# Kernel tuning notes

Measured on AMD Instinct MI355X. Metric: run time of the kernel, lower is better.

## Reference

```python
import jax, jax.numpy as jnp
import numpy as np

NODE_DIM = 128
CTX_DIM = 256
OUT_DIM = 256
GRID_SIZE = 4
SPLINE_ORDER = 3
IN_DIM = 3 * NODE_DIM  # subj + obj + transformed context
N_NODES = 100000
N_EDGES = 100000


def make_grid(in_dim, grid_size, spline_order, grid_range=(-1.0, 1.0)):
    h = (grid_range[1] - grid_range[0]) / grid_size
    g = (np.arange(-spline_order, grid_size + spline_order + 1, dtype=np.float32) * h
         + grid_range[0])  # [grid_size + 2*spline_order + 1]
    return jnp.asarray(np.tile(g[None, :], (in_dim, 1)))  # [in, G]


def b_splines(x, grid, spline_order):
    # x: [N, in], grid: [in, G] -> bases: [N, in, grid_size + spline_order]
    xg = x[:, :, None]
    bases = ((xg >= grid[:, :-1]) & (xg < grid[:, 1:])).astype(x.dtype)
    for k in range(1, spline_order + 1):
        left = (xg - grid[:, : -(k + 1)]) / (grid[:, k:-1] - grid[:, : -(k + 1)]) * bases[..., :-1]
        right = (grid[:, k + 1:] - xg) / (grid[:, k + 1:] - grid[:, 1:-k]) * bases[..., 1:]
        bases = left + right
    return bases


def setup_inputs() -> dict:
    key = jax.random.key(0)
    ks = jax.random.split(key, 8)
    n_coef = GRID_SIZE + SPLINE_ORDER
    return {
        "node_embeddings": jax.random.normal(ks[0], (N_NODES, NODE_DIM), jnp.float32),
        "context_embeddings": jax.random.normal(ks[1], (N_EDGES, CTX_DIM), jnp.float32),
        "pair_indices": jax.random.randint(ks[2], (N_EDGES, 2), 0, N_NODES, jnp.int64 if jax.config.jax_enable_x64 else jnp.int32),
        "ctx_w": jax.random.normal(ks[3], (NODE_DIM, CTX_DIM), jnp.float32) * (1.0 / np.sqrt(CTX_DIM)),
        "ctx_b": jnp.zeros((NODE_DIM,), jnp.float32),
        "base_weight": jax.random.normal(ks[4], (OUT_DIM, IN_DIM), jnp.float32) * (1.0 / np.sqrt(IN_DIM)),
        "spline_weight": jax.random.normal(ks[5], (OUT_DIM, IN_DIM, n_coef), jnp.float32) * 0.1,
        "spline_scaler": jax.random.normal(ks[6], (OUT_DIM, IN_DIM), jnp.float32) * (1.0 / np.sqrt(IN_DIM)),
        "grid": make_grid(IN_DIM, GRID_SIZE, SPLINE_ORDER),
    }


def reference(node_embeddings, context_embeddings, pair_indices, ctx_w, ctx_b,
              base_weight, spline_weight, spline_scaler, grid):
    # gather subject/object node embeddings (irregular access)
    subj = node_embeddings[pair_indices[:, 0]]          # [E, node_dim]
    obj = node_embeddings[pair_indices[:, 1]]           # [E, node_dim]
    ctx = context_embeddings @ ctx_w.T + ctx_b          # [E, node_dim]
    x = jnp.concatenate([subj, obj, ctx], axis=1)       # [E, 3*node_dim]

    # efficient-KAN linear layer: base (SiLU) branch + B-spline branch
    base_out = jax.nn.silu(x) @ base_weight.T           # [E, out]
    bsp = b_splines(x, grid, SPLINE_ORDER)              # [E, in, n_coef]
    scaled_w = spline_weight * spline_scaler[:, :, None]  # [out, in, n_coef]
    spline_out = jnp.einsum('nic,oic->no', bsp, scaled_w)
    return base_out + spline_out
```

## Files before the change

### kernel.cpp

```cpp
#include <hip/hip_runtime.h>

#define NEDGES   100000
#define NODE_DIM 128
#define CTX_DIM  256
#define OUT_DIM  256
#define IN_DIM   384
#define NCOEF    7

#define BM2      128
#define BK2      32
#define NCH2     96
#define THR2     512

typedef __bf16 bf16x8 __attribute__((ext_vector_type(8)));
typedef float  f32x4  __attribute__((ext_vector_type(4)));

static __device__ __forceinline__ unsigned short f2bf(float f) {
    unsigned int u = __float_as_uint(f);
    u += 0x7FFFu + ((u >> 16) & 1u);
    return (unsigned short)(u >> 16);
}
static __device__ __forceinline__ float bf2f(unsigned short h) {
    return __uint_as_float(((unsigned int)h) << 16);
}
static __device__ __forceinline__ unsigned int pkbf(float a, float b) {
    unsigned int ua = __float_as_uint(a), ub = __float_as_uint(b);
    ua += 0x7FFFu + ((ua >> 16) & 1u);
    ub += 0x7FFFu + ((ub >> 16) & 1u);
    return (ua >> 16) | (ub & 0xFFFF0000u);
}
static __device__ __forceinline__ float silu(float x) {
    return x / (1.0f + __expf(-x));
}
static __device__ __forceinline__ float n3(float t) {
    float d2 = t - 2.0f;
    float a  = fabsf(d2);
    float p1 = fmaf(fmaf(0.5f, a, -1.0f), d2 * d2, 0.66666667f);
    float dd = fmaxf(2.0f - a, 0.0f);
    float p2 = dd * dd * (dd * (1.0f / 6.0f));
    return a < 1.0f ? p1 : p2;
}

static __device__ __forceinline__ void glds16(const unsigned short* g, unsigned short* l) {
    __builtin_amdgcn_global_load_lds(
        (const __attribute__((address_space(1))) void*)g,
        (__attribute__((address_space(3))) void*)l, 16, 0, 0);
}

__global__ void prep_w2(const float* __restrict__ base_w,
                        const float* __restrict__ spline_w,
                        const float* __restrict__ spline_s,
                        unsigned short* __restrict__ Wsw)
{
    int o = blockIdx.x;
    int i = threadIdx.x;
    int bi = o * IN_DIM + i;
    float sc = spline_s[bi];
    const float* sw = spline_w + (size_t)bi * NCOEF;
    uint4 v;
    v.x = pkbf(base_w[bi], sw[0] * sc);
    v.y = pkbf(sw[1] * sc, sw[2] * sc);
    v.z = pkbf(sw[3] * sc, sw[4] * sc);
    v.w = pkbf(sw[5] * sc, sw[6] * sc);
    int ch = i >> 2, g8 = i & 3;
    int p  = o * 4 + (((o >> 1) + g8) & 3);
    *(uint4*)(Wsw + (size_t)ch * (OUT_DIM * BK2) + p * 8) = v;
}

__global__ void prep_ctxw(const float* __restrict__ ctx_w,
                          unsigned short* __restrict__ B)
{
    int n  = blockIdx.x;
    int k4 = threadIdx.x;
    float4 v = *(const float4*)(ctx_w + (size_t)n * CTX_DIM + k4 * 4);
    *(uint2*)&B[(size_t)n * CTX_DIM + k4 * 4] =
        make_uint2(pkbf(v.x, v.y), pkbf(v.z, v.w));
}

#define CG_STR 72
#define CG_ESTR 136
__global__ __launch_bounds__(512, 4)
void ctx_gemm(const float* __restrict__ ctx_emb,
              const unsigned short* __restrict__ ctxwB,
              const float* __restrict__ ctx_b,
              unsigned short* __restrict__ CtxB)
{
    __shared__ unsigned short sm[2 * 128 * CG_STR];
    const int tid    = threadIdx.x;
    const int e_base = blockIdx.x * 128;
    const int wid    = tid >> 6;
    const int lan    = tid & 63;
    const int lrow   = lan & 15;
    const int lquad  = lan >> 4;
    const int m0     = (wid & 1) * 64;
    const int n0     = (wid >> 1) * 32;

    f32x4 acc[4][2];
    #pragma unroll
    for (int a = 0; a < 4; ++a)
        #pragma unroll
        for (int b = 0; b < 2; ++b) { f32x4 z = {0.f,0.f,0.f,0.f}; acc[a][b] = z; }

    #pragma unroll
    for (int it = 0; it < 4; ++it) {
        int id = it * 512 + tid;
        int r  = id >> 4;
        int c4 = id & 15;
        int eg = e_base + r; if (eg >= NEDGES) eg = NEDGES - 1;
        float4 v = *(const float4*)(ctx_emb + (size_t)eg * CTX_DIM + c4 * 4);
        *(uint2*)&sm[r * CG_STR + c4 * 4] = make_uint2(pkbf(v.x, v.y), pkbf(v.z, v.w));
    }
    __syncthreads();

    for (int kc = 0; kc < 4; ++kc) {
        if (kc + 1 < 4) {
            unsigned short* nb = sm + ((kc + 1) & 1) * 128 * CG_STR;
            #pragma unroll
            for (int it = 0; it < 4; ++it) {
                int id = it * 512 + tid;
                int r  = id >> 4;
                int c4 = id & 15;
                int eg = e_base + r; if (eg >= NEDGES) eg = NEDGES - 1;
                float4 v = *(const float4*)(ctx_emb + (size_t)eg * CTX_DIM + (kc + 1) * 64 + c4 * 4);
                *(uint2*)&nb[r * CG_STR + c4 * 4] = make_uint2(pkbf(v.x, v.y), pkbf(v.z, v.w));
            }
        }
        const unsigned short* sa = sm + (kc & 1) * 128 * CG_STR;
        #pragma unroll
        for (int ks = 0; ks < 2; ++ks) {
            int koff = ks * 32 + lquad * 8;
            bf16x8 af[4], bfr[2];
            #pragma unroll
            for (int mt = 0; mt < 4; ++mt)
                af[mt] = *(const bf16x8*)&sa[(m0 + mt*16 + lrow) * CG_STR + koff];
            #pragma unroll
            for (int nt = 0; nt < 2; ++nt)
                bfr[nt] = *(const bf16x8*)&ctxwB[(size_t)(n0 + nt*16 + lrow) * CTX_DIM + kc * 64 + koff];
            #pragma unroll
            for (int mt = 0; mt < 4; ++mt)
                #pragma unroll
                for (int nt = 0; nt < 2; ++nt)
                    acc[mt][nt] = __builtin_amdgcn_mfma_f32_16x16x32_bf16(
                        af[mt], bfr[nt], acc[mt][nt], 0, 0, 0);
        }
        __syncthreads();
    }

    #pragma unroll
    for (int nt = 0; nt < 2; ++nt) {
        int col = n0 + nt * 16 + lrow;
        float cb = ctx_b[col];
        #pragma unroll
        for (int mt = 0; mt < 4; ++mt)
            #pragma unroll
            for (int r = 0; r < 4; ++r) {
                int row = m0 + mt * 16 + lquad * 4 + r;
                sm[row * CG_ESTR + col] = f2bf(acc[mt][nt][r] + cb);
            }
    }
    __syncthreads();
    #pragma unroll
    for (int it = 0; it < 8; ++it) {
        int id  = it * 512 + tid;
        int row = id >> 5;
        int g   = id & 31;
        int eg  = e_base + row; if (eg >= NEDGES) eg = NEDGES - 1;
        *(uint2*)&CtxB[(size_t)eg * 128 + g * 4] = *(uint2*)&sm[row * CG_ESTR + g * 4];
    }
}

#define A2STR  40
#define A2SZ   (BM2 * A2STR)
#define B2SZ   (OUT_DIM * BK2)
#define OFF_A0 0
#define OFF_A1 A2SZ
#define OFF_B0 (2 * A2SZ)
#define OFF_B1 (2 * A2SZ + B2SZ)
#define LDS2   (2 * A2SZ + 2 * B2SZ)

static __device__ __forceinline__ void gen_elem(
    float x, float hinv, float b0, unsigned short* dst)
{
    float sl = silu(x);
    unsigned short slh = f2bf(sl);
    float t  = fmaf(x, hinv, b0);
    float jf = floorf(t);
    int   j0 = (int)jf;
    float u  = t - jf;
    float u2 = u * u, u3 = u2 * u;
    float Q0 = u3 * 0.16666667f;
    float d  = 1.0f - u;
    float Q3 = d * d * d * 0.16666667f;
    float Q1 = fmaf(0.5f, u + u2 - u3, 0.16666667f);
    float Q2 = fmaf(0.5f, u3, 0.66666667f - u2);
    unsigned plo = pkbf(Q3, Q2);
    unsigned phi = pkbf(Q1, Q0);
    unsigned long long P = ((unsigned long long)phi << 32) | plo;
    int sh = (j0 << 4) - 32;
    unsigned a  = (unsigned)sh;
    unsigned na = 0u - a;
    unsigned long long lo =
        (a  < 64u) ? (P << (a  & 63u)) : ((na < 64u) ? (P >> (na & 63u)) : 0ull);
    unsigned b2 = a - 64u;
    unsigned nb = 0u - b2;
    unsigned long long hi =
        (b2 < 64u) ? (P << (b2 & 63u)) : ((nb < 64u) ? (P >> (nb & 63u)) : 0ull);
    lo = (lo & ~0xFFFFull) | (unsigned long long)slh;
    uint4 w;
    w.x = (unsigned)lo; w.y = (unsigned)(lo >> 32);
    w.z = (unsigned)hi; w.w = (unsigned)(hi >> 32);
    *(uint4*)dst = w;
}

static __device__ __forceinline__ float fetchx(
    const float* ps, const float* po, const unsigned short* pc, int ch)
{
    if (ch < 32) return ps[ch << 2];
    if (ch < 64) return po[(ch - 32) << 2];
    return bf2f(pc[(ch - 64) << 2]);
}

__global__ __launch_bounds__(THR2, 4)
void kan_gemm2(const unsigned short* __restrict__ Wsw,
               const unsigned short* __restrict__ CtxB,
               const float* __restrict__ node_emb,
               const int*   __restrict__ pair,
               const float* __restrict__ grid,
               float* __restrict__ out)
{
    __shared__ unsigned short smem[LDS2];
    const int tid    = threadIdx.x;
    const int e_base = blockIdx.x * BM2;
    const int wid    = tid >> 6;
    const int lan    = tid & 63;
    const int lrow   = lan & 15;
    const int lquad  = lan >> 4;
    const int m0     = (wid & 1) * 64;
    const int n0     = (wid >> 1) * 64;

    const float g0   = grid[0];
    const float hinv = 1.0f / (grid[1] - grid[0]);
    const float b0   = -g0 * hinv;

    const int grow = tid >> 2;
    const int gcol = tid & 3;
    int geg = e_base + grow; if (geg >= NEDGES) geg = NEDGES - 1;
    const int nsub = pair[geg * 2 + 0];
    const int nobj = pair[geg * 2 + 1];
    const float* ps = node_emb + (size_t)nsub * NODE_DIM + gcol;
    const float* po = node_emb + (size_t)nobj * NODE_DIM + gcol;
    const unsigned short* pc = CtxB + (size_t)geg * 128 + gcol;
    const unsigned awr = grow * A2STR + gcol * 8;

    f32x4 acc[4][4];
    #pragma unroll
    for (int a = 0; a < 4; ++a)
        #pragma unroll
        for (int b = 0; b < 4; ++b) { f32x4 z = {0.f,0.f,0.f,0.f}; acc[a][b] = z; }

    float xc = fetchx(ps, po, pc, 0);
    float xn = fetchx(ps, po, pc, 1);

    #pragma unroll
    for (int it = 0; it < 2; ++it) {
        int id = it * THR2 + tid;
        glds16(Wsw + id * 8, &smem[OFF_B0 + id * 8]);
    }
    gen_elem(xc, hinv, b0, &smem[OFF_A0 + awr]);
    __syncthreads();

    for (int kb = 0; kb < NCH2; ++kb) {
        const int cur = kb & 1;
        if (kb + 1 < NCH2) {
            const unsigned short* wc = Wsw + (size_t)(kb + 1) * B2SZ;
            unsigned boff = cur ? OFF_B0 : OFF_B1;
            #pragma unroll
            for (int it = 0; it < 2; ++it) {
                int id = it * THR2 + tid;
                glds16(wc + id * 8, &smem[boff + id * 8]);
            }
            float xh = xn;
            if (kb + 2 < NCH2) xn = fetchx(ps, po, pc, kb + 2);
            gen_elem(xh, hinv, b0, &smem[(cur ? OFF_A0 : OFF_A1) + awr]);
        }
        const unsigned ab = cur ? OFF_A1 : OFF_A0;
        const unsigned bb = cur ? OFF_B1 : OFF_B0;
        bf16x8 af[4], bfr[4];
        #pragma unroll
        for (int mt = 0; mt < 4; ++mt)
            af[mt] = *(const bf16x8*)&smem[ab + (m0 + mt*16 + lrow) * A2STR + lquad * 8];
        #pragma unroll
        for (int nt = 0; nt < 4; ++nt) {
            int n = n0 + nt * 16 + lrow;
            bfr[nt] = *(const bf16x8*)&smem[bb + n * 32 + ((((n >> 1) + lquad) & 3) << 3)];
        }
        #pragma unroll
        for (int mt = 0; mt < 4; ++mt)
            #pragma unroll
            for (int nt = 0; nt < 4; ++nt)
                acc[mt][nt] = __builtin_amdgcn_mfma_f32_16x16x32_bf16(
                    af[mt], bfr[nt], acc[mt][nt], 0, 0, 0);
        __syncthreads();
    }

    #pragma unroll
    for (int mt = 0; mt < 4; ++mt) {
        #pragma unroll
        for (int r = 0; r < 4; ++r) {
            int row = m0 + mt * 16 + lquad * 4 + r;
            int eg  = e_base + row;
            if (eg < NEDGES) {
                float* op = out + (size_t)eg * OUT_DIM + n0 + lrow;
                #pragma unroll
                for (int nt = 0; nt < 4; ++nt)
                    op[nt * 16] = acc[mt][nt][r];
            }
        }
    }
}

#define XSTR 392
#define FSTR 72
#define FOFF_X 0
#define FOFF_A (128 * XSTR)
#define FOFF_B (FOFF_A + 128 * FSTR)
#define FLDS (FOFF_B + OUT_DIM * FSTR)

__global__ __launch_bounds__(512, 2)
void fused_fallback(const float* __restrict__ node_emb,
                    const float* __restrict__ ctx_emb,
                    const int*   __restrict__ pair,
                    const float* __restrict__ ctx_w,
                    const float* __restrict__ ctx_b,
                    const float* __restrict__ base_w,
                    const float* __restrict__ spline_w,
                    const float* __restrict__ spline_s,
                    const float* __restrict__ grid,
                    float* __restrict__ out)
{
    __shared__ unsigned short smem[FLDS];
    const int tid    = threadIdx.x;
    const int e_base = blockIdx.x * 128;
    const int wid    = tid >> 6;
    const int lan    = tid & 63;
    const int lrow   = lan & 15;
    const int lquad  = lan >> 4;

    #pragma unroll
    for (int it = 0; it < 16; ++it) {
        int id    = it * 512 + tid;
        int lane4 = id & 31;
        int e     = (id >> 5) & 127;
        int which = id >> 12;
        int eg = e_base + e; if (eg >= NEDGES) eg = NEDGES - 1;
        int node = pair[eg * 2 + which];
        const float4 v = *(const float4*)(node_emb + (size_t)node * NODE_DIM + lane4 * 4);
        *(ushort4*)&smem[FOFF_X + e * XSTR + which * NODE_DIM + lane4 * 4] =
            make_ushort4(f2bf(v.x), f2bf(v.y), f2bf(v.z), f2bf(v.w));
    }
    {
        f32x4 cacc[4][2];
        #pragma unroll
        for (int a = 0; a < 4; ++a)
            #pragma unroll
            for (int b = 0; b < 2; ++b) { f32x4 z = {0.f,0.f,0.f,0.f}; cacc[a][b] = z; }
        const int m0 = (wid & 1) * 64;
        const int n0 = (wid >> 1) * 32;
        for (int kc = 0; kc < 4; ++kc) {
            #pragma unroll
            for (int it = 0; it < 4; ++it) {
                int id = it * 512 + tid;
                int r  = id >> 4;
                int c4 = id & 15;
                int eg = e_base + r; if (eg >= NEDGES) eg = NEDGES - 1;
                float4 v = *(const float4*)(ctx_emb + (size_t)eg * CTX_DIM + kc * 64 + c4 * 4);
                *(ushort4*)&smem[FOFF_A + r * FSTR + c4 * 4] =
                    make_ushort4(f2bf(v.x), f2bf(v.y), f2bf(v.z), f2bf(v.w));
                float4 w = *(const float4*)(ctx_w + (size_t)r * CTX_DIM + kc * 64 + c4 * 4);
                *(ushort4*)&smem[FOFF_B + r * FSTR + c4 * 4] =
                    make_ushort4(f2bf(w.x), f2bf(w.y), f2bf(w.z), f2bf(w.w));
            }
            __syncthreads();
            #pragma unroll
            for (int ks = 0; ks < 2; ++ks) {
                int koff = ks * 32 + lquad * 8;
                bf16x8 af[4], bfr[2];
                #pragma unroll
                for (int mt = 0; mt < 4; ++mt)
                    af[mt] = *(const bf16x8*)&smem[FOFF_A + (m0 + mt*16 + lrow) * FSTR + koff];
                #pragma unroll
                for (int nt = 0; nt < 2; ++nt)
                    bfr[nt] = *(const bf16x8*)&smem[FOFF_B + (n0 + nt*16 + lrow) * FSTR + koff];
                #pragma unroll
                for (int mt = 0; mt < 4; ++mt)
                    #pragma unroll
                    for (int nt = 0; nt < 2; ++nt)
                        cacc[mt][nt] = __builtin_amdgcn_mfma_f32_16x16x32_bf16(
                            af[mt], bfr[nt], cacc[mt][nt], 0, 0, 0);
            }
            __syncthreads();
        }
        #pragma unroll
        for (int mt = 0; mt < 4; ++mt)
            #pragma unroll
            for (int nt = 0; nt < 2; ++nt)
                #pragma unroll
                for (int r = 0; r < 4; ++r) {
                    int row = m0 + mt*16 + lquad*4 + r;
                    int col = n0 + nt*16 + lrow;
                    smem[FOFF_X + row * XSTR + 256 + col] = f2bf(cacc[mt][nt][r] + ctx_b[col]);
                }
    }
    __syncthreads();

    const float g0   = grid[0];
    const float hinv = 1.0f / (grid[1] - grid[0]);

    f32x4 acc[4][4];
    #pragma unroll
    for (int a = 0; a < 4; ++a)
        #pragma unroll
        for (int b = 0; b < 4; ++b) { f32x4 z = {0.f,0.f,0.f,0.f}; acc[a][b] = z; }

    const int m0 = (wid & 1) * 64;
    const int n0 = (wid >> 1) * 64;

    for (int kb = 0; kb < 48; ++kb) {
        const int seg = kb / 6;
        const int i0  = (kb - seg * 6) * 64;
        #pragma unroll
        for (int it = 0; it < 4; ++it) {
            int id = it * 512 + tid;
            int e  = id >> 4;
            int qq = id & 15;
            ushort4 xv = *(const ushort4*)&smem[FOFF_X + e * XSTR + i0 + qq * 4];
            float x0 = bf2f(xv.x), x1 = bf2f(xv.y), x2 = bf2f(xv.z), x3 = bf2f(xv.w);
            unsigned short r0, r1, r2, r3;
            if (seg == 0) {
                r0 = f2bf(silu(x0)); r1 = f2bf(silu(x1));
                r2 = f2bf(silu(x2)); r3 = f2bf(silu(x3));
            } else {
                const float cf = (float)(seg - 1);
                r0 = f2bf(n3((x0 - g0) * hinv - cf));
                r1 = f2bf(n3((x1 - g0) * hinv - cf));
                r2 = f2bf(n3((x2 - g0) * hinv - cf));
                r3 = f2bf(n3((x3 - g0) * hinv - cf));
            }
            *(ushort4*)&smem[FOFF_A + e * FSTR + qq * 4] = make_ushort4(r0, r1, r2, r3);
        }
        #pragma unroll
        for (int it = 0; it < 4; ++it) {
            int id = it * 512 + tid;
            int o  = id >> 4;
            int qq = id & 15;
            unsigned short r0, r1, r2, r3;
            if (seg == 0) {
                const float4 w = *(const float4*)(base_w + (size_t)o * IN_DIM + i0 + qq * 4);
                r0 = f2bf(w.x); r1 = f2bf(w.y); r2 = f2bf(w.z); r3 = f2bf(w.w);
            } else {
                int c  = seg - 1;
                int bi = o * IN_DIM + i0 + qq * 4;
                r0 = f2bf(spline_w[(size_t)(bi    ) * NCOEF + c] * spline_s[bi    ]);
                r1 = f2bf(spline_w[(size_t)(bi + 1) * NCOEF + c] * spline_s[bi + 1]);
                r2 = f2bf(spline_w[(size_t)(bi + 2) * NCOEF + c] * spline_s[bi + 2]);
                r3 = f2bf(spline_w[(size_t)(bi + 3) * NCOEF + c] * spline_s[bi + 3]);
            }
            *(ushort4*)&smem[FOFF_B + o * FSTR + qq * 4] = make_ushort4(r0, r1, r2, r3);
        }
        __syncthreads();
        #pragma unroll
        for (int ks = 0; ks < 2; ++ks) {
            int koff = ks * 32 + lquad * 8;
            bf16x8 af[4], bfr[4];
            #pragma unroll
            for (int mt = 0; mt < 4; ++mt)
                af[mt] = *(const bf16x8*)&smem[FOFF_A + (m0 + mt*16 + lrow) * FSTR + koff];
            #pragma unroll
            for (int nt = 0; nt < 4; ++nt)
                bfr[nt] = *(const bf16x8*)&smem[FOFF_B + (n0 + nt*16 + lrow) * FSTR + koff];
            #pragma unroll
            for (int mt = 0; mt < 4; ++mt)
                #pragma unroll
                for (int nt = 0; nt < 4; ++nt)
                    acc[mt][nt] = __builtin_amdgcn_mfma_f32_16x16x32_bf16(
                        af[mt], bfr[nt], acc[mt][nt], 0, 0, 0);
        }
        __syncthreads();
    }

    #pragma unroll
    for (int mt = 0; mt < 4; ++mt) {
        #pragma unroll
        for (int r = 0; r < 4; ++r) {
            int row = m0 + mt*16 + lquad*4 + r;
            int eg  = e_base + row;
            if (eg < NEDGES) {
                float* op = out + (size_t)eg * OUT_DIM + n0 + lrow;
                #pragma unroll
                for (int nt = 0; nt < 4; ++nt)
                    op[nt * 16] = acc[mt][nt][r];
            }
        }
    }
}

extern "C" void kernel_launch(void* const* d_in, const int* in_sizes, int n_in,
                              void* d_out, int out_size, void* d_ws, size_t ws_size,
                              hipStream_t stream)
{
    const float* node_emb = (const float*)d_in[0];
    const float* ctx_emb  = (const float*)d_in[1];
    const int*   pair     = (const int*)d_in[2];
    const float* ctx_w    = (const float*)d_in[3];
    const float* ctx_b    = (const float*)d_in[4];
    const float* base_w   = (const float*)d_in[5];
    const float* spline_w = (const float*)d_in[6];
    const float* spline_s = (const float*)d_in[7];
    const float* grid     = (const float*)d_in[8];
    float* out = (float*)d_out;

    const int nblk = (NEDGES + BM2 - 1) / BM2;
    const size_t ctxwoff = 1572864u;
    const size_t xoff    = 2u * 1024u * 1024u;
    const size_t need = xoff + (size_t)NEDGES * 128 * sizeof(unsigned short);

    if (ws_size >= need) {
        unsigned short* Wsw   = (unsigned short*)d_ws;
        unsigned short* CtxwB = (unsigned short*)((char*)d_ws + ctxwoff);
        unsigned short* CtxB  = (unsigned short*)((char*)d_ws + xoff);
        prep_w2<<<OUT_DIM, IN_DIM, 0, stream>>>(base_w, spline_w, spline_s, Wsw);
        prep_ctxw<<<128, 64, 0, stream>>>(ctx_w, CtxwB);
        ctx_gemm<<<nblk, 512, 0, stream>>>(ctx_emb, CtxwB, ctx_b, CtxB);
        kan_gemm2<<<nblk, THR2, 0, stream>>>(Wsw, CtxB, node_emb, pair, grid, out);
    } else {
        fused_fallback<<<nblk, 512, 0, stream>>>(
            node_emb, ctx_emb, pair, ctx_w, ctx_b, base_w, spline_w, spline_s, grid, out);
    }
}
```

Measured before the change: 446.1 us.

## Fuse context projection GEMM into KAN GEMM kernel prologue

Moves the context-embedding projection GEMM into the start of the main KAN GEMM kernel, so each block computes its own 128 rows of the bf16 context slice before the main loop. This removes one kernel launch and the inter-kernel boundary. The result is still written to global memory and then re-read through the existing fetch path. The change also moves the next x fetch ahead of the weight prefetch issue. The risk is longer per-block latency and higher register pressure in the main kernel.

```diff
diff --git a/kernel.cpp b/kernel.cpp
--- a/kernel.cpp
+++ b/kernel.cpp
@@ -77,98 +77,6 @@
         make_uint2(pkbf(v.x, v.y), pkbf(v.z, v.w));
 }
 
-#define CG_STR 72
-#define CG_ESTR 136
-__global__ __launch_bounds__(512, 4)
-void ctx_gemm(const float* __restrict__ ctx_emb,
-              const unsigned short* __restrict__ ctxwB,
-              const float* __restrict__ ctx_b,
-              unsigned short* __restrict__ CtxB)
-{
-    __shared__ unsigned short sm[2 * 128 * CG_STR];
-    const int tid    = threadIdx.x;
-    const int e_base = blockIdx.x * 128;
-    const int wid    = tid >> 6;
-    const int lan    = tid & 63;
-    const int lrow   = lan & 15;
-    const int lquad  = lan >> 4;
-    const int m0     = (wid & 1) * 64;
-    const int n0     = (wid >> 1) * 32;
-
-    f32x4 acc[4][2];
-    #pragma unroll
-    for (int a = 0; a < 4; ++a)
-        #pragma unroll
-        for (int b = 0; b < 2; ++b) { f32x4 z = {0.f,0.f,0.f,0.f}; acc[a][b] = z; }
-
-    #pragma unroll
-    for (int it = 0; it < 4; ++it) {
-        int id = it * 512 + tid;
-        int r  = id >> 4;
-        int c4 = id & 15;
-        int eg = e_base + r; if (eg >= NEDGES) eg = NEDGES - 1;
-        float4 v = *(const float4*)(ctx_emb + (size_t)eg * CTX_DIM + c4 * 4);
-        *(uint2*)&sm[r * CG_STR + c4 * 4] = make_uint2(pkbf(v.x, v.y), pkbf(v.z, v.w));
-    }
-    __syncthreads();
-
-    for (int kc = 0; kc < 4; ++kc) {
-        if (kc + 1 < 4) {
-            unsigned short* nb = sm + ((kc + 1) & 1) * 128 * CG_STR;
-            #pragma unroll
-            for (int it = 0; it < 4; ++it) {
-                int id = it * 512 + tid;
-                int r  = id >> 4;
-                int c4 = id & 15;
-                int eg = e_base + r; if (eg >= NEDGES) eg = NEDGES - 1;
-                float4 v = *(const float4*)(ctx_emb + (size_t)eg * CTX_DIM + (kc + 1) * 64 + c4 * 4);
-                *(uint2*)&nb[r * CG_STR + c4 * 4] = make_uint2(pkbf(v.x, v.y), pkbf(v.z, v.w));
-            }
-        }
-        const unsigned short* sa = sm + (kc & 1) * 128 * CG_STR;
-        #pragma unroll
-        for (int ks = 0; ks < 2; ++ks) {
-            int koff = ks * 32 + lquad * 8;
-            bf16x8 af[4], bfr[2];
-            #pragma unroll
-            for (int mt = 0; mt < 4; ++mt)
-                af[mt] = *(const bf16x8*)&sa[(m0 + mt*16 + lrow) * CG_STR + koff];
-            #pragma unroll
-            for (int nt = 0; nt < 2; ++nt)
-                bfr[nt] = *(const bf16x8*)&ctxwB[(size_t)(n0 + nt*16 + lrow) * CTX_DIM + kc * 64 + koff];
-            #pragma unroll
-            for (int mt = 0; mt < 4; ++mt)
-                #pragma unroll
-                for (int nt = 0; nt < 2; ++nt)
-                    acc[mt][nt] = __builtin_amdgcn_mfma_f32_16x16x32_bf16(
-                        af[mt], bfr[nt], acc[mt][nt], 0, 0, 0);
-        }
-        __syncthreads();
-    }
-
-    #pragma unroll
-    for (int nt = 0; nt < 2; ++nt) {
-        int col = n0 + nt * 16 + lrow;
-        float cb = ctx_b[col];
-        #pragma unroll
-        for (int mt = 0; mt < 4; ++mt)
-            #pragma unroll
-            for (int r = 0; r < 4; ++r) {
-                int row = m0 + mt * 16 + lquad * 4 + r;
-                sm[row * CG_ESTR + col] = f2bf(acc[mt][nt][r] + cb);
-            }
-    }
-    __syncthreads();
-    #pragma unroll
-    for (int it = 0; it < 8; ++it) {
-        int id  = it * 512 + tid;
-        int row = id >> 5;
-        int g   = id & 31;
-        int eg  = e_base + row; if (eg >= NEDGES) eg = NEDGES - 1;
-        *(uint2*)&CtxB[(size_t)eg * 128 + g * 4] = *(uint2*)&sm[row * CG_ESTR + g * 4];
-    }
-}
-
 #define A2STR  40
 #define A2SZ   (BM2 * A2STR)
 #define B2SZ   (OUT_DIM * BK2)
@@ -177,6 +85,8 @@
 #define OFF_B0 (2 * A2SZ)
 #define OFF_B1 (2 * A2SZ + B2SZ)
 #define LDS2   (2 * A2SZ + 2 * B2SZ)
+#define CG_STR 72
+#define CG_ESTR 136
 
 static __device__ __forceinline__ void gen_elem(
     float x, float hinv, float b0, unsigned short* dst)
@@ -222,7 +132,10 @@
 
 __global__ __launch_bounds__(THR2, 4)
 void kan_gemm2(const unsigned short* __restrict__ Wsw,
-               const unsigned short* __restrict__ CtxB,
+               const float* __restrict__ ctx_emb,
+               const unsigned short* __restrict__ ctxwB,
+               const float* __restrict__ ctx_b,
+               unsigned short* __restrict__ CtxB,
                const float* __restrict__ node_emb,
                const int*   __restrict__ pair,
                const float* __restrict__ grid,
@@ -238,6 +151,83 @@
     const int m0     = (wid & 1) * 64;
     const int n0     = (wid >> 1) * 64;
 
+    {
+        f32x4 cacc[4][2];
+        #pragma unroll
+        for (int a = 0; a < 4; ++a)
+            #pragma unroll
+            for (int b = 0; b < 2; ++b) { f32x4 z = {0.f,0.f,0.f,0.f}; cacc[a][b] = z; }
+        const int cn0 = (wid >> 1) * 32;
+
+        #pragma unroll
+        for (int it = 0; it < 4; ++it) {
+            int id = it * THR2 + tid;
+            int r  = id >> 4;
+            int c4 = id & 15;
+            int eg = e_base + r; if (eg >= NEDGES) eg = NEDGES - 1;
+            float4 v = *(const float4*)(ctx_emb + (size_t)eg * CTX_DIM + c4 * 4);
+            *(uint2*)&smem[r * CG_STR + c4 * 4] = make_uint2(pkbf(v.x, v.y), pkbf(v.z, v.w));
+        }
+        __syncthreads();
+
+        for (int kc = 0; kc < 4; ++kc) {
+            if (kc + 1 < 4) {
+                unsigned short* nb = smem + ((kc + 1) & 1) * (128 * CG_STR);
+                #pragma unroll
+                for (int it = 0; it < 4; ++it) {
+                    int id = it * THR2 + tid;
+                    int r  = id >> 4;
+                    int c4 = id & 15;
+                    int eg = e_base + r; if (eg >= NEDGES) eg = NEDGES - 1;
+                    float4 v = *(const float4*)(ctx_emb + (size_t)eg * CTX_DIM + (kc + 1) * 64 + c4 * 4);
+                    *(uint2*)&nb[r * CG_STR + c4 * 4] = make_uint2(pkbf(v.x, v.y), pkbf(v.z, v.w));
+                }
+            }
+            const unsigned short* sa = smem + (kc & 1) * (128 * CG_STR);
+            #pragma unroll
+            for (int ks = 0; ks < 2; ++ks) {
+                int koff = ks * 32 + lquad * 8;
+                bf16x8 caf[4], cbf[2];
+                #pragma unroll
+                for (int mt = 0; mt < 4; ++mt)
+                    caf[mt] = *(const bf16x8*)&sa[(m0 + mt*16 + lrow) * CG_STR + koff];
+                #pragma unroll
+                for (int nt = 0; nt < 2; ++nt)
+                    cbf[nt] = *(const bf16x8*)&ctxwB[(size_t)(cn0 + nt*16 + lrow) * CTX_DIM + kc * 64 + koff];
+                #pragma unroll
+                for (int mt = 0; mt < 4; ++mt)
+                    #pragma unroll
+                    for (int nt = 0; nt < 2; ++nt)
+                        cacc[mt][nt] = __builtin_amdgcn_mfma_f32_16x16x32_bf16(
+                            caf[mt], cbf[nt], cacc[mt][nt], 0, 0, 0);
+            }
+            __syncthreads();
+        }
+
+        #pragma unroll
+        for (int nt = 0; nt < 2; ++nt) {
+            int col = cn0 + nt * 16 + lrow;
+            float cb = ctx_b[col];
+            #pragma unroll
+            for (int mt = 0; mt < 4; ++mt)
+                #pragma unroll
+                for (int r = 0; r < 4; ++r) {
+                    int row = m0 + mt * 16 + lquad * 4 + r;
+                    smem[row * CG_ESTR + col] = f2bf(cacc[mt][nt][r] + cb);
+                }
+        }
+        __syncthreads();
+        #pragma unroll
+        for (int it = 0; it < 8; ++it) {
+            int id  = it * THR2 + tid;
+            int row = id >> 5;
+            int g   = id & 31;
+            int eg  = e_base + row; if (eg >= NEDGES) eg = NEDGES - 1;
+            *(uint2*)&CtxB[(size_t)eg * 128 + g * 4] = *(uint2*)&smem[row * CG_ESTR + g * 4];
+        }
+        __syncthreads();
+    }
+
     const float g0   = grid[0];
     const float hinv = 1.0f / (grid[1] - grid[0]);
     const float b0   = -g0 * hinv;
@@ -272,6 +262,8 @@
     for (int kb = 0; kb < NCH2; ++kb) {
         const int cur = kb & 1;
         if (kb + 1 < NCH2) {
+            float xh = xn;
+            if (kb + 2 < NCH2) xn = fetchx(ps, po, pc, kb + 2);
             const unsigned short* wc = Wsw + (size_t)(kb + 1) * B2SZ;
             unsigned boff = cur ? OFF_B0 : OFF_B1;
             #pragma unroll
@@ -279,8 +271,6 @@
                 int id = it * THR2 + tid;
                 glds16(wc + id * 8, &smem[boff + id * 8]);
             }
-            float xh = xn;
-            if (kb + 2 < NCH2) xn = fetchx(ps, po, pc, kb + 2);
             gen_elem(xh, hinv, b0, &smem[(cur ? OFF_A0 : OFF_A1) + awr]);
         }
         const unsigned ab = cur ? OFF_A1 : OFF_A0;
@@ -530,8 +520,8 @@
         unsigned short* CtxB  = (unsigned short*)((char*)d_ws + xoff);
         prep_w2<<<OUT_DIM, IN_DIM, 0, stream>>>(base_w, spline_w, spline_s, Wsw);
         prep_ctxw<<<128, 64, 0, stream>>>(ctx_w, CtxwB);
-        ctx_gemm<<<nblk, 512, 0, stream>>>(ctx_emb, CtxwB, ctx_b, CtxB);
-        kan_gemm2<<<nblk, THR2, 0, stream>>>(Wsw, CtxB, node_emb, pair, grid, out);
+        kan_gemm2<<<nblk, THR2, 0, stream>>>(
+            Wsw, ctx_emb, CtxwB, ctx_b, CtxB, node_emb, pair, grid, out);
     } else {
         fused_fallback<<<nblk, 512, 0, stream>>>(
             node_emb, ctx_emb, pair, ctx_w, ctx_b, base_w, spline_w, spline_s, grid, out);
```

New measurement: 435.4 us. 2.4% less time.
